# Optimization experiments

Hardware: AMD Instinct MI355X
Metric: run time of the kernel (lower is better)

Reference implementation:

```python
import jax, jax.numpy as jnp
import numpy as np

DIM = 4096
KROT = 8
GROUP = 128
NG = DIM // GROUP  # 32 groups
N = 16384          # tokens


def setup_inputs() -> dict:
    key = jax.random.key(0)
    kx, kt, ks = jax.random.split(key, 3)
    x = jax.random.normal(kx, (N, DIM), dtype=jnp.float32)
    theta = jax.random.normal(kt, (KROT, DIM // 2), dtype=jnp.float32) * 0.1
    # pairs: for each krot layer, a permutation of [0, GROUP) tiled across groups
    rng = np.random.default_rng(0)
    pairs = np.stack([
        np.tile(rng.permutation(GROUP).astype(np.int32), NG) for _ in range(KROT)
    ])  # [KROT, DIM], local (within-group) indices
    channel_scales = jax.random.uniform(ks, (1, DIM), dtype=jnp.float32,
                                        minval=0.5, maxval=1.5)
    return {"x": x, "pairs": jnp.asarray(pairs), "theta": theta,
            "channel_scales": channel_scales}


def reference(x, pairs, theta, channel_scales):
    # global channel offset for each position of the tiled permutation
    off = jnp.repeat(jnp.arange(NG, dtype=jnp.int32) * GROUP, GROUP)  # [DIM]
    for k in range(KROT):
        idx = pairs[k] + off          # [DIM] global channel indices (a permutation)
        ie = idx[0::2]                # [DIM//2] first element of each Givens pair
        io = idx[1::2]                # [DIM//2] second element
        a = x[:, ie]                  # [N, DIM//2]
        b = x[:, io]
        c = jnp.cos(theta[k])         # [DIM//2]
        s = jnp.sin(theta[k])
        x = x.at[:, ie].set(a * c - b * s).at[:, io].set(a * s + b * c)
    return x * channel_scales
```

## Files before the change

### kernel.cpp

```cpp
#include <hip/hip_runtime.h>
#include <hip/hip_bf16.h>

#define DIMX  4096
#define KROT  8
#define GRP   128
#define NGG   32
#define NROWS 16384
#define RT2   64
#define NT2   (NROWS / RT2)
#define GPG   24
#define GRID2 (NGG * GPG)

typedef float f32x4 __attribute__((ext_vector_type(4)));
typedef short s16x8 __attribute__((ext_vector_type(8)));
typedef unsigned short u16;

__global__ __launch_bounds__(512) void compose(const float* __restrict__ theta,
                                               const int*   __restrict__ pairs,
                                               const float* __restrict__ scales,
                                               u16* __restrict__ B) {
    __shared__ float M[GRP * GRP];
    const int g = blockIdx.x;
    const int tid = threadIdx.x;
    const int j = tid & 127, q = tid >> 7;

    for (int r = q * 32; r < q * 32 + 32; ++r) M[r * GRP + j] = (r == j) ? 1.f : 0.f;
    __syncthreads();

    for (int k = 0; k < KROT; ++k) {
        for (int t = 0; t < 16; ++t) {
            int tp = q * 16 + t;
            int ie = pairs[k * DIMX + g * GRP + 2 * tp];
            int io = pairs[k * DIMX + g * GRP + 2 * tp + 1];
            float ang = theta[k * (DIMX / 2) + g * 64 + tp];
            float c = cosf(ang), s = sinf(ang);
            float a = M[ie * GRP + j], b = M[io * GRP + j];
            M[ie * GRP + j] = a * c - b * s;
            M[io * GRP + j] = a * s + b * c;
        }
        __syncthreads();
    }

    const int l = tid & 63, nt = (tid >> 6) & 1, ks = (tid >> 7) & 3;
    for (int w = 0; w < 4; ++w) {
        int c = w * 32 + nt * 16 + (l & 15);
        float sc = scales[g * GRP + c];
        int dbase = ks * 32 + ((l >> 4) & 3) * 8;
        s16x8 vh, vl;
        #pragma unroll
        for (int e = 0; e < 8; ++e) {
            float v = sc * M[c * GRP + dbase + e];
            __hip_bfloat16 h = __float2bfloat16(v);
            float r = v - __bfloat162float(h);
            __hip_bfloat16 lo = __float2bfloat16(r);
            vh[e] = (short)*(u16*)&h;
            vl[e] = (short)*(u16*)&lo;
        }
        int off = (((g * 4 + w) * 4 + ks) * 2 + nt) * 2;
        *(s16x8*)(B + (size_t)(off + 0) * 512 + l * 8) = vh;
        *(s16x8*)(B + (size_t)(off + 1) * 512 + l * 8) = vl;
    }
}

__global__ __launch_bounds__(256, 3) void rot_gemm(const float* __restrict__ x,
                                                   const u16* __restrict__ B,
                                                   float* __restrict__ out) {
    __shared__ __align__(16) float C[RT2 * GRP];
    const int tid = threadIdx.x;
    const int l  = tid & 63, wv = tid >> 6;
    const int lr = l & 15;
    const int lq = (l >> 4) & 3;
    const int g  = blockIdx.x & 31;

    s16x8 bh[4][2], bl[4][2];
    #pragma unroll
    for (int ks = 0; ks < 4; ++ks)
        #pragma unroll
        for (int nt = 0; nt < 2; ++nt) {
            int off = (((g * 4 + wv) * 4 + ks) * 2 + nt) * 2;
            bh[ks][nt] = *(const s16x8*)(B + (size_t)(off + 0) * 512 + l * 8);
            bl[ks][nt] = *(const s16x8*)(B + (size_t)(off + 1) * 512 + l * 8);
        }

    for (int rt = blockIdx.x >> 5; rt < NT2; rt += GPG) {
        const float* xt = x + (size_t)(rt * RT2) * DIMX + g * GRP;
        f32x4 acc[4][2] = {};

        #pragma unroll 1
        for (int m = 0; m < 4; ++m) {
            f32x4 a0[4], a1[4];
            #pragma unroll
            for (int ks = 0; ks < 4; ++ks) {
                const float* p = xt + (size_t)(m * 16 + lr) * DIMX + ks * 32 + lq * 8;
                a0[ks] = *(const f32x4*)p;
                a1[ks] = *(const f32x4*)(p + 4);
            }
            #pragma unroll
            for (int ks = 0; ks < 4; ++ks) {
                s16x8 ah, al;
                #pragma unroll
                for (int e = 0; e < 8; ++e) {
                    float v = (e < 4) ? a0[ks][e] : a1[ks][e - 4];
                    unsigned u = __builtin_bit_cast(unsigned, v);
                    ah[e] = (short)(u >> 16);
                    float r = v - __builtin_bit_cast(float, u & 0xffff0000u);
                    __hip_bfloat16 lo = __float2bfloat16(r);
                    al[e] = (short)*(u16*)&lo;
                }
                #pragma unroll
                for (int nt = 0; nt < 2; ++nt) {
                    acc[m][nt] = __builtin_amdgcn_mfma_f32_16x16x32_bf16(ah, bh[ks][nt], acc[m][nt], 0, 0, 0);
                    acc[m][nt] = __builtin_amdgcn_mfma_f32_16x16x32_bf16(ah, bl[ks][nt], acc[m][nt], 0, 0, 0);
                    acc[m][nt] = __builtin_amdgcn_mfma_f32_16x16x32_bf16(al, bh[ks][nt], acc[m][nt], 0, 0, 0);
                }
            }
        }

        #pragma unroll
        for (int m = 0; m < 4; ++m)
            #pragma unroll
            for (int nt = 0; nt < 2; ++nt)
                #pragma unroll
                for (int i = 0; i < 4; ++i) {
                    int row = m * 16 + lq * 4 + i;
                    int col = wv * 32 + nt * 16 + lr;
                    C[row * GRP + (col ^ ((row & 12) << 2))] = acc[m][nt][i];
                }
        __syncthreads();

        float* ob = out + (size_t)(rt * RT2) * DIMX + g * GRP;
        #pragma unroll
        for (int j = 0; j < 8; ++j) {
            int flat = j * 256 + tid;
            int row = flat >> 5, c4 = (flat & 31) * 4;
            f32x4 v = *(const f32x4*)&C[row * GRP + (c4 ^ ((row & 12) << 2))];
            *(f32x4*)(ob + (size_t)row * DIMX + c4) = v;
        }
        __syncthreads();
    }
}

extern "C" void kernel_launch(void* const* d_in, const int* in_sizes, int n_in,
                              void* d_out, int out_size, void* d_ws, size_t ws_size,
                              hipStream_t stream) {
    const float* xin    = (const float*)d_in[0];
    const int*   pairs  = (const int*)d_in[1];
    const float* theta  = (const float*)d_in[2];
    const float* scales = (const float*)d_in[3];
    float* outp = (float*)d_out;
    u16*   Btab = (u16*)d_ws;

    compose<<<NGG, 512, 0, stream>>>(theta, pairs, scales, Btab);
    rot_gemm<<<GRID2, 256, 0, stream>>>(xin, Btab, outp);
}
```

Baseline: 508.2 us.

## Double-buffer x tile loads, pack bf16 split conversion, raise occupancy

Each 16-row x slab is now prefetched into a second register buffer while the MFMAs for the current slab run. The m loop is fully unrolled. The hi/lo bf16 split of x switches from truncation plus per-element conversion to paired round-to-nearest conversion (__float22bfloat162_rn). Launch bounds go from 3 to 4 blocks per SM and the grid grows from 24 to 32 row-groups per column group, aiming to hide global-load latency with more overlap and occupancy, at the cost of extra register pressure that could cause spills.

```diff
diff --git a/kernel.cpp b/kernel.cpp
--- a/kernel.cpp
+++ b/kernel.cpp
@@ -8,11 +8,13 @@
 #define NROWS 16384
 #define RT2   64
 #define NT2   (NROWS / RT2)
-#define GPG   24
+#define GPG   32
 #define GRID2 (NGG * GPG)
 
 typedef float f32x4 __attribute__((ext_vector_type(4)));
 typedef short s16x8 __attribute__((ext_vector_type(8)));
+typedef unsigned int u32;
+typedef u32 u32x4 __attribute__((ext_vector_type(4)));
 typedef unsigned short u16;
 
 __global__ __launch_bounds__(512) void compose(const float* __restrict__ theta,
@@ -53,8 +55,11 @@
             __hip_bfloat16 h = __float2bfloat16(v);
             float r = v - __bfloat162float(h);
             __hip_bfloat16 lo = __float2bfloat16(r);
-            vh[e] = (short)*(u16*)&h;
-            vl[e] = (short)*(u16*)&lo;
+            u16 hb, lb2;
+            __builtin_memcpy(&hb, &h, 2);
+            __builtin_memcpy(&lb2, &lo, 2);
+            vh[e] = (short)hb;
+            vl[e] = (short)lb2;
         }
         int off = (((g * 4 + w) * 4 + ks) * 2 + nt) * 2;
         *(s16x8*)(B + (size_t)(off + 0) * 512 + l * 8) = vh;
@@ -62,7 +67,7 @@
     }
 }
 
-__global__ __launch_bounds__(256, 3) void rot_gemm(const float* __restrict__ x,
+__global__ __launch_bounds__(256, 4) void rot_gemm(const float* __restrict__ x,
                                                    const u16* __restrict__ B,
                                                    float* __restrict__ out) {
     __shared__ __align__(16) float C[RT2 * GRP];
@@ -84,29 +89,46 @@
 
     for (int rt = blockIdx.x >> 5; rt < NT2; rt += GPG) {
         const float* xt = x + (size_t)(rt * RT2) * DIMX + g * GRP;
+        f32x4 A0[2][4], A1[2][4];
+
+        #pragma unroll
+        for (int ks = 0; ks < 4; ++ks) {
+            const float* p = xt + (size_t)(0 * 16 + lr) * DIMX + ks * 32 + lq * 8;
+            A0[0][ks] = *(const f32x4*)p;
+            A1[0][ks] = *(const f32x4*)(p + 4);
+        }
+
         f32x4 acc[4][2] = {};
-
-        #pragma unroll 1
+        #pragma unroll
         for (int m = 0; m < 4; ++m) {
-            f32x4 a0[4], a1[4];
-            #pragma unroll
-            for (int ks = 0; ks < 4; ++ks) {
-                const float* p = xt + (size_t)(m * 16 + lr) * DIMX + ks * 32 + lq * 8;
-                a0[ks] = *(const f32x4*)p;
-                a1[ks] = *(const f32x4*)(p + 4);
+            const int cur = m & 1, nxt = cur ^ 1;
+            if (m < 3) {
+                #pragma unroll
+                for (int ks = 0; ks < 4; ++ks) {
+                    const float* p = xt + (size_t)((m + 1) * 16 + lr) * DIMX + ks * 32 + lq * 8;
+                    A0[nxt][ks] = *(const f32x4*)p;
+                    A1[nxt][ks] = *(const f32x4*)(p + 4);
+                }
             }
             #pragma unroll
             for (int ks = 0; ks < 4; ++ks) {
-                s16x8 ah, al;
+                u32x4 hd, ld;
                 #pragma unroll
-                for (int e = 0; e < 8; ++e) {
-                    float v = (e < 4) ? a0[ks][e] : a1[ks][e - 4];
-                    unsigned u = __builtin_bit_cast(unsigned, v);
-                    ah[e] = (short)(u >> 16);
-                    float r = v - __builtin_bit_cast(float, u & 0xffff0000u);
-                    __hip_bfloat16 lo = __float2bfloat16(r);
-                    al[e] = (short)*(u16*)&lo;
+                for (int j = 0; j < 4; ++j) {
+                    float v0 = (j < 2) ? A0[cur][ks][2 * j]     : A1[cur][ks][2 * j - 4];
+                    float v1 = (j < 2) ? A0[cur][ks][2 * j + 1] : A1[cur][ks][2 * j - 3];
+                    __hip_bfloat162 hb = __float22bfloat162_rn(make_float2(v0, v1));
+                    float r0 = v0 - __bfloat162float(hb.x);
+                    float r1 = v1 - __bfloat162float(hb.y);
+                    __hip_bfloat162 lb = __float22bfloat162_rn(make_float2(r0, r1));
+                    u32 hw, lw;
+                    __builtin_memcpy(&hw, &hb, 4);
+                    __builtin_memcpy(&lw, &lb, 4);
+                    hd[j] = hw;
+                    ld[j] = lw;
                 }
+                s16x8 ah = __builtin_bit_cast(s16x8, hd);
+                s16x8 al = __builtin_bit_cast(s16x8, ld);
                 #pragma unroll
                 for (int nt = 0; nt < 2; ++nt) {
                     acc[m][nt] = __builtin_amdgcn_mfma_f32_16x16x32_bf16(ah, bh[ks][nt], acc[m][nt], 0, 0, 0);
```

After: 711.7 us. 40.0% more time.
